# Kernel optimization log

Measured on AMD Instinct MI355X. Metric: run time of the kernel, lower is better.

## Reference

```python
import jax, jax.numpy as jnp
import numpy as np

C = 512
NUM_HEADS = 8
HEAD_DIM = 64
GROUPS = 32
EPS = 1e-5


def setup_inputs() -> dict:
    key = jax.random.key(0)
    ks = jax.random.split(key, 7)
    x = jax.random.normal(ks[0], (2, C, 64, 64), dtype=jnp.float32)
    norm_w = jnp.ones((C,), jnp.float32)
    norm_b = jnp.zeros((C,), jnp.float32)
    s1 = 1.0 / np.sqrt(C)
    qkv_w = jax.random.uniform(ks[1], (3 * C, C), jnp.float32, -s1, s1)
    qkv_b = jax.random.uniform(ks[2], (3 * C,), jnp.float32, -s1, s1)
    proj_w = jax.random.uniform(ks[3], (C, C), jnp.float32, -s1, s1)
    proj_b = jax.random.uniform(ks[4], (C,), jnp.float32, -s1, s1)
    return {"x": x, "norm_w": norm_w, "norm_b": norm_b,
            "qkv_w": qkv_w, "qkv_b": qkv_b,
            "proj_w": proj_w, "proj_b": proj_b}


def reference(x, norm_w, norm_b, qkv_w, qkv_b, proj_w, proj_b):
    b, c, h, w = x.shape
    n = h * w
    x_flat = x.reshape(b, c, n)
    # GroupNorm(32, C): stats over (channels-in-group, spatial)
    xg = x_flat.reshape(b, GROUPS, c // GROUPS, n)
    mean = xg.mean(axis=(2, 3), keepdims=True)
    var = xg.var(axis=(2, 3), keepdims=True)
    hn = ((xg - mean) * jax.lax.rsqrt(var + EPS)).reshape(b, c, n)
    hn = hn * norm_w[None, :, None] + norm_b[None, :, None]
    # 1x1 conv QKV = matmul over channel dim
    qkv = jnp.einsum('oc,bcn->bon', qkv_w, hn) + qkv_b[None, :, None]
    q, k, v = jnp.split(qkv, 3, axis=1)
    q = q.reshape(b, NUM_HEADS, HEAD_DIM, n)
    k = k.reshape(b, NUM_HEADS, HEAD_DIM, n)
    v = v.reshape(b, NUM_HEADS, HEAD_DIM, n)
    scale = HEAD_DIM ** (-0.5)
    attn = jnp.einsum('bhdn,bhdm->bhnm', q, k) * scale  # [b,H,N,N]
    attn = jax.nn.softmax(attn, axis=-1)
    out = jnp.einsum('bhnm,bhdm->bhdn', attn, v).reshape(b, c, n)
    out = jnp.einsum('oc,bcn->bon', proj_w, out) + proj_b[None, :, None]
    return (x_flat + out).reshape(b, c, h, w)
```

## Files before the change

### kernel.cpp

```cpp
#include <hip/hip_runtime.h>
#include <hip/hip_bf16.h>
#include <math.h>

#define BATCH 2
#define CCH   512
#define NSP   4096
#define NHEAD 8
#define HDIM  64
#define NGRP  32
#define CPG   16
#define EPSV  1e-5f
#define NSPLIT 2
#define MTN   (NSP / NSPLIT / 64)
#define SMSCALE 0.1803368801111204f

typedef __attribute__((ext_vector_type(8))) short short8;
typedef __attribute__((ext_vector_type(4))) short short4v;
typedef __attribute__((ext_vector_type(4))) float f32x4;
typedef __hip_bfloat16 bf16;

static __device__ __forceinline__ unsigned pk2(float a, float b) {
    return ((__float_as_uint(a) + 0x8000u) >> 16) |
           ((__float_as_uint(b) + 0x8000u) & 0xFFFF0000u);
}
static __device__ __forceinline__ unsigned pk1(float a) {
    return (__float_as_uint(a) + 0x8000u) >> 16;
}
static __device__ __forceinline__ float upk(unsigned u) {
    unsigned v = u << 16;
    return __uint_as_float(v);
}
static __device__ __forceinline__ float fexp2(float x) {
    return __builtin_amdgcn_exp2f(x);
}
static __device__ __forceinline__ void gload16(const bf16* g, bf16* l) {
    __builtin_amdgcn_global_load_lds(
        (const __attribute__((address_space(1))) unsigned*)g,
        (__attribute__((address_space(3))) unsigned*)l, 16, 0, 0);
}

__global__ __launch_bounds__(256) void prep0(const float* __restrict__ x,
                                             const float* __restrict__ qkvw,
                                             const float* __restrict__ pw,
                                             float* __restrict__ sbuf,
                                             bf16* __restrict__ wq, bf16* __restrict__ wp) {
    if (blockIdx.x < 1024) {
        const int bg = blockIdx.x >> 4, sub = blockIdx.x & 15;
        const float4* p = (const float4*)(x + (size_t)bg * (CPG * NSP)) +
                          (size_t)sub * (CPG * NSP / 4 / 16);
        float s = 0.f, ss = 0.f;
#pragma unroll
        for (int it = 0; it < 4; it++) {
            float4 v = p[it * 256 + threadIdx.x];
            s  += v.x + v.y + v.z + v.w;
            ss += v.x * v.x + v.y * v.y + v.z * v.z + v.w * v.w;
        }
        for (int o = 32; o > 0; o >>= 1) {
            s  += __shfl_down(s, o);
            ss += __shfl_down(ss, o);
        }
        __shared__ float shs[4], shss[4];
        const int wid = threadIdx.x >> 6, lane = threadIdx.x & 63;
        if (lane == 0) { shs[wid] = s; shss[wid] = ss; }
        __syncthreads();
        if (threadIdx.x == 0) {
            s  = shs[0] + shs[1] + shs[2] + shs[3];
            ss = shss[0] + shss[1] + shss[2] + shss[3];
            sbuf[bg * 16 + sub]        = s;
            sbuf[1024 + bg * 16 + sub] = ss;
        }
    } else {
        const int i = (blockIdx.x - 1024) * 256 + threadIdx.x;
        const int NQ = 1536 * 512 / 4;
        float4 v; bf16* dst; int di;
        if (i < NQ) { v = ((const float4*)qkvw)[i]; dst = wq; di = i; }
        else        { v = ((const float4*)pw)[i - NQ]; dst = wp; di = i - NQ; }
        uint2 o = {pk2(v.x, v.y), pk2(v.z, v.w)};
        *(uint2*)(dst + (size_t)di * 4) = o;
    }
}

__global__ __launch_bounds__(256) void gn_apply_t(const float* __restrict__ x,
                                                  const float* __restrict__ sbuf,
                                                  const float* __restrict__ nw,
                                                  const float* __restrict__ nb,
                                                  bf16* __restrict__ hnt) {
    __shared__ float Ls[64][68];
    __shared__ float Gmu[4], Grs[4];
    const int b  = blockIdx.z;
    const int c0 = blockIdx.y * 64;
    const int n0 = blockIdx.x * 64;
    const int t  = threadIdx.x;
    const int cl = t >> 4, n4 = (t & 15) * 4;
    if (t < 4) {
        const int bg = b * NGRP + (c0 >> 4) + t;
        float s = 0.f, ss = 0.f;
#pragma unroll
        for (int i = 0; i < 16; i++) {
            s  += sbuf[bg * 16 + i];
            ss += sbuf[1024 + bg * 16 + i];
        }
        const float invn = 1.f / (float)(CPG * NSP);
        const float mu = s * invn;
        Gmu[t] = mu;
        Grs[t] = rsqrtf(ss * invn - mu * mu + EPSV);
    }
    __syncthreads();
#pragma unroll
    for (int ph = 0; ph < 4; ph++) {
        const int c  = c0 + ph * 16 + cl;
        const float mu = Gmu[ph], rs = Grs[ph];
        const float sw = nw[c] * rs;
        const float sb = nb[c] - mu * sw;
        float4 v = *(const float4*)&x[((size_t)b * CCH + c) * NSP + n0 + n4];
        float4 o;
        o.x = v.x * sw + sb; o.y = v.y * sw + sb;
        o.z = v.z * sw + sb; o.w = v.w * sw + sb;
        *(float4*)&Ls[ph * 16 + cl][n4] = o;
    }
    __syncthreads();
#pragma unroll
    for (int ph = 0; ph < 2; ph++) {
        const int task = ph * 256 + t;
        const int nl = task & 63, cc = (task >> 6) * 8;
        uint4 o;
        o.x = pk2(Ls[cc + 0][nl], Ls[cc + 1][nl]);
        o.y = pk2(Ls[cc + 2][nl], Ls[cc + 3][nl]);
        o.z = pk2(Ls[cc + 4][nl], Ls[cc + 5][nl]);
        o.w = pk2(Ls[cc + 6][nl], Ls[cc + 7][nl]);
        *(uint4*)&hnt[((size_t)b * NSP + n0 + nl) * CCH + c0 + cc] = o;
    }
}

#define GEMM_STAGE(CUR)                                         \
    gload16(aSrc0, &As[CUR][(wave * 16) * 32]);                 \
    gload16(aSrc1, &As[CUR][(64 + wave * 16) * 32]);            \
    gload16(bSrc0, &Bs[CUR][(wave * 16) * 32]);                 \
    gload16(bSrc1, &Bs[CUR][(64 + wave * 16) * 32]);            \
    aSrc0 += 32; aSrc1 += 32; bSrc0 += 32; bSrc1 += 32;

#define GEMM_MAIN(Wptr, Xptr)                                                            \
    __shared__ __align__(16) bf16 As[2][128 * 32];                                       \
    __shared__ __align__(16) bf16 Bs[2][128 * 32];                                       \
    const int t = threadIdx.x, wave = t >> 6, lane = t & 63;                             \
    const int quad = lane >> 4, l15 = lane & 15;                                         \
    const int srow = lane >> 2, scol = (lane & 3) * 8;                                   \
    const int b   = blockIdx.z;                                                          \
    const int wm = wave >> 1, wn = wave & 1;                                             \
    const int m0w = blockIdx.y * 128 + wm * 64;                                          \
    const int n0w = blockIdx.x * 128 + wn * 64;                                          \
    const bf16* aSrc0 = Wptr + (size_t)(blockIdx.y * 128 + wave * 16 + srow) * 512 + scol; \
    const bf16* aSrc1 = aSrc0 + (size_t)64 * 512;                                        \
    const bf16* bSrc0 = Xptr + ((size_t)b * NSP + blockIdx.x * 128 + wave * 16 + srow) * 512 + scol; \
    const bf16* bSrc1 = bSrc0 + (size_t)64 * 512;                                        \
    f32x4 acc[4][4];                                                                     \
    _Pragma("unroll")                                                                    \
    for (int i = 0; i < 4; i++)                                                          \
        _Pragma("unroll")                                                                \
        for (int j = 0; j < 4; j++) acc[i][j] = (f32x4){0.f, 0.f, 0.f, 0.f};             \
    GEMM_STAGE(0)                                                                        \
    __syncthreads();                                                                     \
    _Pragma("unroll")                                                                    \
    for (int ks = 0; ks < 16; ks++) {                                                    \
        const int cur = ks & 1;                                                          \
        if (ks < 15) { GEMM_STAGE(cur ^ 1) }                                             \
        short8 af[4], bfr[4];                                                            \
        _Pragma("unroll")                                                                \
        for (int mf = 0; mf < 4; mf++)                                                   \
            af[mf] = *(const short8*)&As[cur][(wm * 64 + mf * 16 + l15) * 32 + quad * 8]; \
        _Pragma("unroll")                                                                \
        for (int nf = 0; nf < 4; nf++)                                                   \
            bfr[nf] = *(const short8*)&Bs[cur][(wn * 64 + nf * 16 + l15) * 32 + quad * 8]; \
        _Pragma("unroll")                                                                \
        for (int mf = 0; mf < 4; mf++)                                                   \
            _Pragma("unroll")                                                            \
            for (int nf = 0; nf < 4; nf++)                                               \
                acc[mf][nf] = __builtin_amdgcn_mfma_f32_16x16x32_bf16(af[mf], bfr[nf],   \
                                                                      acc[mf][nf], 0, 0, 0); \
        __syncthreads();                                                                 \
    }

__global__ __launch_bounds__(256) void gemm_qkv(const bf16* __restrict__ Wb,
                                                const bf16* __restrict__ Xt,
                                                const float* __restrict__ bias,
                                                bf16* __restrict__ qt, bf16* __restrict__ kt,
                                                bf16* __restrict__ vt) {
    GEMM_MAIN(Wb, Xt)

    const int sec = m0w >> 9, h = (m0w >> 6) & 7, bh = b * NHEAD + h;
    const float sm = (sec == 0) ? SMSCALE : 1.0f;
    float bi[4][4];
#pragma unroll
    for (int mf = 0; mf < 4; mf++)
#pragma unroll
        for (int r = 0; r < 4; r++) bi[mf][r] = bias[m0w + mf * 16 + quad * 4 + r];

    if (sec < 2) {
        bf16* dst = (sec == 0) ? qt : kt;
#pragma unroll
        for (int mf = 0; mf < 4; mf++)
#pragma unroll
            for (int nf = 0; nf < 4; nf++) {
                const int n = n0w + nf * 16 + l15;
                float v0 = (acc[mf][nf][0] + bi[mf][0]) * sm;
                float v1 = (acc[mf][nf][1] + bi[mf][1]) * sm;
                float v2 = (acc[mf][nf][2] + bi[mf][2]) * sm;
                float v3 = (acc[mf][nf][3] + bi[mf][3]) * sm;
                uint2 o = {pk2(v0, v1), pk2(v2, v3)};
                *(uint2*)(dst + ((size_t)bh * NSP + n) * HDIM + mf * 16 + quad * 4) = o;
            }
    } else {
#pragma unroll
        for (int mf = 0; mf < 4; mf++)
#pragma unroll
            for (int nf = 0; nf < 4; nf++)
#pragma unroll
                for (int r = 0; r < 4; r++) {
                    const float v = acc[mf][nf][r] + bi[mf][r];
                    const int n = n0w + nf * 16 + l15;
                    const int d = mf * 16 + quad * 4 + r;
                    unsigned u = pk1(v);
                    vt[((size_t)bh * HDIM + d) * NSP + n] = *(bf16*)&u;
                }
    }
}

__global__ __launch_bounds__(256) void gemm_proj(const bf16* __restrict__ Wb,
                                                 const bf16* __restrict__ Xt,
                                                 const float* __restrict__ bias,
                                                 const float* __restrict__ resid,
                                                 float* __restrict__ out) {
    GEMM_MAIN(Wb, Xt)

    float bi[4][4];
#pragma unroll
    for (int mf = 0; mf < 4; mf++)
#pragma unroll
        for (int r = 0; r < 4; r++) bi[mf][r] = bias[m0w + mf * 16 + quad * 4 + r];

    float* scratch = (float*)As;
    const int n0 = blockIdx.x * 128;
#pragma unroll
    for (int p = 0; p < 4; p++) {
        if (wm == (p >> 1)) {
#pragma unroll
            for (int ml = 0; ml < 2; ml++) {
                const int mf = (p & 1) * 2 + ml;
#pragma unroll
                for (int nf = 0; nf < 4; nf++)
#pragma unroll
                    for (int r = 0; r < 4; r++)
                        scratch[(ml * 16 + quad * 4 + r) * 128 + wn * 64 + nf * 16 + l15] =
                            acc[mf][nf][r] + bi[mf][r];
            }
        }
        __syncthreads();
#pragma unroll
        for (int i = 0; i < 4; i++) {
            const int idx = i * 256 + t;
            const int row = idx >> 5, c4 = idx & 31;
            const int m = blockIdx.y * 128 + p * 32 + row;
            const size_t off = ((size_t)b * CCH + m) * NSP + n0 + c4 * 4;
            float4 rv = *(const float4*)&resid[off];
            float4 sv = *(const float4*)&scratch[row * 128 + c4 * 4];
            float4 ov;
            ov.x = sv.x + rv.x; ov.y = sv.y + rv.y;
            ov.z = sv.z + rv.z; ov.w = sv.w + rv.w;
            *(float4*)&out[off] = ov;
        }
        __syncthreads();
    }
}

__global__ __launch_bounds__(256, 2) void attn10(const bf16* __restrict__ qt,
                                                 const bf16* __restrict__ kt,
                                                 const bf16* __restrict__ vt,
                                                 bf16* __restrict__ opart,
                                                 float* __restrict__ lpart) {
    __shared__ __align__(16) bf16 Ks[2][64][68];
    __shared__ __align__(16) bf16 Vs[2][64][68];
    const int t = threadIdx.x, wave = t >> 6, lane = t & 63;
    const int quad = lane >> 4, l15 = lane & 15;
    const int blk = blockIdx.x;
    const int xcd = blk & 7, slot = blk >> 3;
    const int qtile = slot & 15;
    const int grp = xcd + 8 * (slot >> 4);
    const int spl = grp & 1, bh = grp >> 1;
    const int b = bh >> 3, h = bh & 7;
    const int qb  = qtile * 256 + wave * 64;
    const int kb0 = spl * (NSP / NSPLIT);

    const bf16* Qb = qt + (size_t)bh * NSP * HDIM;

    const int trow = t >> 3;
    const int tcol = (t & 7) * 8;
    const bf16* kSrcA = kt + (size_t)bh * NSP * HDIM + (size_t)(kb0 + trow) * HDIM + tcol;
    const bf16* kSrcB = kSrcA + 32 * HDIM;
    const bf16* vSrcA = vt + (size_t)bh * HDIM * NSP + (size_t)trow * NSP + kb0 + tcol;
    const bf16* vSrcB = vSrcA + (size_t)32 * NSP;

    short8 qf[4][2];
#pragma unroll
    for (int qs = 0; qs < 4; qs++)
#pragma unroll
        for (int c = 0; c < 2; c++)
            qf[qs][c] = *(const short8*)(Qb + (size_t)(qb + qs * 16 + l15) * HDIM + c * 32 + quad * 8);

    short8 onesf;
    {
        const short one = (short)0x3F80;
        short8 o1 = {one, one, one, one, one, one, one, one};
        short8 zz = {0, 0, 0, 0, 0, 0, 0, 0};
        onesf = (l15 == 0) ? o1 : zz;
    }

    f32x4 o[4][4], ol[4];
#pragma unroll
    for (int qs = 0; qs < 4; qs++) {
        ol[qs] = (f32x4){0.f, 0.f, 0.f, 0.f};
#pragma unroll
        for (int ds = 0; ds < 4; ds++) o[qs][ds] = (f32x4){0.f, 0.f, 0.f, 0.f};
    }

    uint4 rKA, rKB, rVA, rVB;
#define ATTN_LOAD()                                         \
    rKA = *(const uint4*)kSrcA; kSrcA += 64 * HDIM;         \
    rKB = *(const uint4*)kSrcB; kSrcB += 64 * HDIM;         \
    rVA = *(const uint4*)vSrcA; vSrcA += 64;                \
    rVB = *(const uint4*)vSrcB; vSrcB += 64;
#define ATTN_STAGE(BUF)                                     \
    *(uint4*)&Ks[BUF][trow][tcol] = rKA;                    \
    *(uint4*)&Ks[BUF][32 + trow][tcol] = rKB;               \
    *(uint4*)&Vs[BUF][trow][tcol] = rVA;                    \
    *(uint4*)&Vs[BUF][32 + trow][tcol] = rVB;
#define ATTN_COMPUTE(BUF)                                                                \
    {                                                                                    \
        short8 kf[4][2], vf[4][2];                                                       \
        _Pragma("unroll")                                                                \
        for (int ms = 0; ms < 4; ms++)                                                   \
            _Pragma("unroll")                                                            \
            for (int c = 0; c < 2; c++)                                                  \
                kf[ms][c] = *(const short8*)&Ks[BUF][ms * 16 + l15][c * 32 + quad * 8];  \
        _Pragma("unroll")                                                                \
        for (int ds = 0; ds < 4; ds++)                                                   \
            _Pragma("unroll")                                                            \
            for (int c = 0; c < 2; c++)                                                  \
                vf[ds][c] = *(const short8*)&Vs[BUF][ds * 16 + l15][c * 32 + quad * 8];  \
        _Pragma("unroll")                                                                \
        for (int qs = 0; qs < 4; qs++) {                                                 \
            f32x4 s[4];                                                                  \
            __builtin_amdgcn_s_setprio(1);                                               \
            _Pragma("unroll")                                                            \
            for (int ms = 0; ms < 4; ms++) {                                             \
                f32x4 a = (f32x4){0.f, 0.f, 0.f, 0.f};                                   \
                a = __builtin_amdgcn_mfma_f32_16x16x32_bf16(kf[ms][0], qf[qs][0], a, 0, 0, 0); \
                a = __builtin_amdgcn_mfma_f32_16x16x32_bf16(kf[ms][1], qf[qs][1], a, 0, 0, 0); \
                s[ms] = a;                                                               \
            }                                                                            \
            __builtin_amdgcn_s_setprio(0);                                               \
            unsigned rr[4][2];                                                           \
            _Pragma("unroll")                                                            \
            for (int ms = 0; ms < 4; ms++) {                                             \
                float e0 = fexp2(s[ms][0]);                                              \
                float e1 = fexp2(s[ms][1]);                                              \
                float e2 = fexp2(s[ms][2]);                                              \
                float e3 = fexp2(s[ms][3]);                                              \
                asm("v_cvt_pk_bf16_f32 %0, %1, %2" : "=v"(rr[ms][0]) : "v"(e0), "v"(e1)); \
                asm("v_cvt_pk_bf16_f32 %0, %1, %2" : "=v"(rr[ms][1]) : "v"(e2), "v"(e3)); \
            }                                                                            \
            _Pragma("unroll")                                                            \
            for (int j = 0; j < 2; j++) {                                                \
                asm("v_permlane32_swap_b32 %0, %1" : "+v"(rr[0][j]), "+v"(rr[1][j]));    \
                asm("v_permlane32_swap_b32 %0, %1" : "+v"(rr[2][j]), "+v"(rr[3][j]));    \
            }                                                                            \
            _Pragma("unroll")                                                            \
            for (int j = 0; j < 2; j++) {                                                \
                asm("v_permlane16_swap_b32 %0, %1" : "+v"(rr[0][j]), "+v"(rr[1][j]));    \
                asm("v_permlane16_swap_b32 %0, %1" : "+v"(rr[2][j]), "+v"(rr[3][j]));    \
            }                                                                            \
            short8 pf0, pf1;                                                             \
            {                                                                            \
                unsigned* p0 = (unsigned*)&pf0;                                          \
                p0[0] = rr[0][0]; p0[1] = rr[0][1]; p0[2] = rr[1][0]; p0[3] = rr[1][1];  \
                unsigned* p1 = (unsigned*)&pf1;                                          \
                p1[0] = rr[2][0]; p1[1] = rr[2][1]; p1[2] = rr[3][0]; p1[3] = rr[3][1];  \
            }                                                                            \
            __builtin_amdgcn_s_setprio(1);                                               \
            _Pragma("unroll")                                                            \
            for (int ds = 0; ds < 4; ds++) {                                             \
                f32x4 a = o[qs][ds];                                                     \
                a = __builtin_amdgcn_mfma_f32_16x16x32_bf16(pf0, vf[ds][0], a, 0, 0, 0); \
                a = __builtin_amdgcn_mfma_f32_16x16x32_bf16(pf1, vf[ds][1], a, 0, 0, 0); \
                o[qs][ds] = a;                                                           \
            }                                                                            \
            {                                                                            \
                f32x4 a = ol[qs];                                                        \
                a = __builtin_amdgcn_mfma_f32_16x16x32_bf16(pf0, onesf, a, 0, 0, 0);     \
                a = __builtin_amdgcn_mfma_f32_16x16x32_bf16(pf1, onesf, a, 0, 0, 0);     \
                ol[qs] = a;                                                              \
            }                                                                            \
            __builtin_amdgcn_s_setprio(0);                                               \
        }                                                                                \
    }

    ATTN_LOAD()
    ATTN_STAGE(0)
    ATTN_LOAD()
    __syncthreads();

    for (int mt = 0; mt < MTN; mt += 2) {
        ATTN_STAGE(1)
        ATTN_LOAD()
        ATTN_COMPUTE(0)
        __syncthreads();
        ATTN_STAGE(0)
        ATTN_LOAD()
        ATTN_COMPUTE(1)
        __syncthreads();
    }
#undef ATTN_LOAD
#undef ATTN_STAGE
#undef ATTN_COMPUTE

#pragma unroll
    for (int qs = 0; qs < 4; qs++) {
#pragma unroll
        for (int ds = 0; ds < 4; ds++)
#pragma unroll
            for (int r = 0; r < 4; r++) {
                const int q = qb + qs * 16 + quad * 4 + r;
                unsigned u = pk1(o[qs][ds][r]);
                opart[((size_t)(spl * BATCH + b) * NSP + q) * CCH + h * 64 + ds * 16 + l15] =
                    *(bf16*)&u;
            }
        if (l15 == 0) {
#pragma unroll
            for (int r = 0; r < 4; r++) {
                const int q = qb + qs * 16 + quad * 4 + r;
                lpart[(((size_t)spl * BATCH + b) * NHEAD + h) * NSP + q] = ol[qs][r];
            }
        }
    }
}

__global__ __launch_bounds__(256) void attn_combine(const bf16* __restrict__ opart,
                                                    const float* __restrict__ lpart,
                                                    bf16* __restrict__ att_t) {
    const int idx = blockIdx.x * 256 + threadIdx.x;
    const int c8 = (idx & 63) * 8;
    const int n  = (idx >> 6) & 4095;
    const int b  = idx >> 18;
    const int h  = c8 >> 6;
    float l = 0.f;
#pragma unroll
    for (int s = 0; s < NSPLIT; s++)
        l += lpart[(((size_t)s * BATCH + b) * NHEAD + h) * NSP + n];
    const float inv = 1.f / l;
    float acc[8] = {};
#pragma unroll
    for (int s = 0; s < NSPLIT; s++) {
        uint4 u = *(const uint4*)&opart[((size_t)(s * BATCH + b) * NSP + n) * CCH + c8];
        acc[0] += upk(u.x); acc[1] += upk(u.x >> 16);
        acc[2] += upk(u.y); acc[3] += upk(u.y >> 16);
        acc[4] += upk(u.z); acc[5] += upk(u.z >> 16);
        acc[6] += upk(u.w); acc[7] += upk(u.w >> 16);
    }
    uint4 o;
    o.x = pk2(acc[0] * inv, acc[1] * inv);
    o.y = pk2(acc[2] * inv, acc[3] * inv);
    o.z = pk2(acc[4] * inv, acc[5] * inv);
    o.w = pk2(acc[6] * inv, acc[7] * inv);
    *(uint4*)&att_t[((size_t)b * NSP + n) * CCH + c8] = o;
}

extern "C" void kernel_launch(void* const* d_in, const int* in_sizes, int n_in,
                              void* d_out, int out_size, void* d_ws, size_t ws_size,
                              hipStream_t stream) {
    const float* x    = (const float*)d_in[0];
    const float* nw   = (const float*)d_in[1];
    const float* nb   = (const float*)d_in[2];
    const float* qkvw = (const float*)d_in[3];
    const float* qkvb = (const float*)d_in[4];
    const float* pw   = (const float*)d_in[5];
    const float* pb   = (const float*)d_in[6];
    float* out = (float*)d_out;
    char* ws   = (char*)d_ws;

    float* sbuf = (float*)ws;
    bf16* wq  = (bf16*)(ws + (size_t)1  * 1024 * 1024);
    bf16* wp  = (bf16*)(ws + (size_t)3  * 1024 * 1024);
    bf16* hnt = (bf16*)(ws + (size_t)4  * 1024 * 1024);
    bf16* qtb = (bf16*)(ws + (size_t)12 * 1024 * 1024);
    bf16* ktb = (bf16*)(ws + (size_t)20 * 1024 * 1024);
    bf16* vtb = (bf16*)(ws + (size_t)28 * 1024 * 1024);
    bf16* opart = (bf16*)(ws + (size_t)36 * 1024 * 1024);
    float* lpart = (float*)(ws + (size_t)56 * 1024 * 1024);
    bf16* att = hnt;

    hipLaunchKernelGGL(prep0, dim3(1024 + 1024), dim3(256), 0, stream,
                       x, qkvw, pw, sbuf, wq, wp);
    hipLaunchKernelGGL(gn_apply_t, dim3(NSP / 64, CCH / 64, BATCH), dim3(256), 0, stream,
                       x, sbuf, nw, nb, hnt);
    hipLaunchKernelGGL(gemm_qkv, dim3(NSP / 128, 1536 / 128, BATCH), dim3(256), 0, stream,
                       wq, hnt, qkvb, qtb, ktb, vtb);
    hipLaunchKernelGGL(attn10, dim3(512), dim3(256), 0, stream,
                       qtb, ktb, vtb, opart, lpart);
    hipLaunchKernelGGL(attn_combine, dim3(BATCH * NSP * CCH / 8 / 256), dim3(256), 0, stream,
                       opart, lpart, att);
    hipLaunchKernelGGL(gemm_proj, dim3(NSP / 128, CCH / 128, BATCH), dim3(256), 0, stream,
                       wp, att, pb, x, out);
}
```

Measured before the change: 201.8 us.

## Fuse split-attention combine into projection GEMM B-operand load

Removes the separate attn_combine kernel and instead has gemm_proj read both split partial outputs and their softmax denominators, combine and normalize them in registers, and write the bf16 result directly into the shared-memory B tile. The combined attention tensor no longer makes a round trip through global memory and one launch is dropped. In exchange, each proj block redoes the combine for its tile across all four M-blocks, so opart is read repeatedly. The B operand also switches from async global-to-LDS loads to register loads with explicit writes, which may add latency to the GEMM pipeline.

New measurement: 203.8 us. Within noise of the previous version (+1.0%).

```diff
diff --git a/kernel.cpp b/kernel.cpp
--- a/kernel.cpp
+++ b/kernel.cpp
@@ -139,53 +139,50 @@
     gload16(bSrc1, &Bs[CUR][(64 + wave * 16) * 32]);            \
     aSrc0 += 32; aSrc1 += 32; bSrc0 += 32; bSrc1 += 32;
 
-#define GEMM_MAIN(Wptr, Xptr)                                                            \
-    __shared__ __align__(16) bf16 As[2][128 * 32];                                       \
-    __shared__ __align__(16) bf16 Bs[2][128 * 32];                                       \
-    const int t = threadIdx.x, wave = t >> 6, lane = t & 63;                             \
-    const int quad = lane >> 4, l15 = lane & 15;                                         \
-    const int srow = lane >> 2, scol = (lane & 3) * 8;                                   \
-    const int b   = blockIdx.z;                                                          \
-    const int wm = wave >> 1, wn = wave & 1;                                             \
-    const int m0w = blockIdx.y * 128 + wm * 64;                                          \
-    const int n0w = blockIdx.x * 128 + wn * 64;                                          \
-    const bf16* aSrc0 = Wptr + (size_t)(blockIdx.y * 128 + wave * 16 + srow) * 512 + scol; \
-    const bf16* aSrc1 = aSrc0 + (size_t)64 * 512;                                        \
-    const bf16* bSrc0 = Xptr + ((size_t)b * NSP + blockIdx.x * 128 + wave * 16 + srow) * 512 + scol; \
-    const bf16* bSrc1 = bSrc0 + (size_t)64 * 512;                                        \
-    f32x4 acc[4][4];                                                                     \
-    _Pragma("unroll")                                                                    \
-    for (int i = 0; i < 4; i++)                                                          \
-        _Pragma("unroll")                                                                \
-        for (int j = 0; j < 4; j++) acc[i][j] = (f32x4){0.f, 0.f, 0.f, 0.f};             \
-    GEMM_STAGE(0)                                                                        \
-    __syncthreads();                                                                     \
-    _Pragma("unroll")                                                                    \
-    for (int ks = 0; ks < 16; ks++) {                                                    \
-        const int cur = ks & 1;                                                          \
-        if (ks < 15) { GEMM_STAGE(cur ^ 1) }                                             \
-        short8 af[4], bfr[4];                                                            \
-        _Pragma("unroll")                                                                \
-        for (int mf = 0; mf < 4; mf++)                                                   \
-            af[mf] = *(const short8*)&As[cur][(wm * 64 + mf * 16 + l15) * 32 + quad * 8]; \
-        _Pragma("unroll")                                                                \
-        for (int nf = 0; nf < 4; nf++)                                                   \
-            bfr[nf] = *(const short8*)&Bs[cur][(wn * 64 + nf * 16 + l15) * 32 + quad * 8]; \
-        _Pragma("unroll")                                                                \
-        for (int mf = 0; mf < 4; mf++)                                                   \
-            _Pragma("unroll")                                                            \
-            for (int nf = 0; nf < 4; nf++)                                               \
-                acc[mf][nf] = __builtin_amdgcn_mfma_f32_16x16x32_bf16(af[mf], bfr[nf],   \
-                                                                      acc[mf][nf], 0, 0, 0); \
-        __syncthreads();                                                                 \
-    }
-
 __global__ __launch_bounds__(256) void gemm_qkv(const bf16* __restrict__ Wb,
                                                 const bf16* __restrict__ Xt,
                                                 const float* __restrict__ bias,
                                                 bf16* __restrict__ qt, bf16* __restrict__ kt,
                                                 bf16* __restrict__ vt) {
-    GEMM_MAIN(Wb, Xt)
+    __shared__ __align__(16) bf16 As[2][128 * 32];
+    __shared__ __align__(16) bf16 Bs[2][128 * 32];
+    const int t = threadIdx.x, wave = t >> 6, lane = t & 63;
+    const int quad = lane >> 4, l15 = lane & 15;
+    const int srow = lane >> 2, scol = (lane & 3) * 8;
+    const int b   = blockIdx.z;
+    const int wm = wave >> 1, wn = wave & 1;
+    const int m0w = blockIdx.y * 128 + wm * 64;
+    const int n0w = blockIdx.x * 128 + wn * 64;
+    const bf16* aSrc0 = Wb + (size_t)(blockIdx.y * 128 + wave * 16 + srow) * 512 + scol;
+    const bf16* aSrc1 = aSrc0 + (size_t)64 * 512;
+    const bf16* bSrc0 = Xt + ((size_t)b * NSP + blockIdx.x * 128 + wave * 16 + srow) * 512 + scol;
+    const bf16* bSrc1 = bSrc0 + (size_t)64 * 512;
+    f32x4 acc[4][4];
+#pragma unroll
+    for (int i = 0; i < 4; i++)
+#pragma unroll
+        for (int j = 0; j < 4; j++) acc[i][j] = (f32x4){0.f, 0.f, 0.f, 0.f};
+    GEMM_STAGE(0)
+    __syncthreads();
+#pragma unroll
+    for (int ks = 0; ks < 16; ks++) {
+        const int cur = ks & 1;
+        if (ks < 15) { GEMM_STAGE(cur ^ 1) }
+        short8 af[4], bfr[4];
+#pragma unroll
+        for (int mf = 0; mf < 4; mf++)
+            af[mf] = *(const short8*)&As[cur][(wm * 64 + mf * 16 + l15) * 32 + quad * 8];
+#pragma unroll
+        for (int nf = 0; nf < 4; nf++)
+            bfr[nf] = *(const short8*)&Bs[cur][(wn * 64 + nf * 16 + l15) * 32 + quad * 8];
+#pragma unroll
+        for (int mf = 0; mf < 4; mf++)
+#pragma unroll
+            for (int nf = 0; nf < 4; nf++)
+                acc[mf][nf] = __builtin_amdgcn_mfma_f32_16x16x32_bf16(af[mf], bfr[nf],
+                                                                      acc[mf][nf], 0, 0, 0);
+        __syncthreads();
+    }
 
     const int sec = m0w >> 9, h = (m0w >> 6) & 7, bh = b * NHEAD + h;
     const float sm = (sec == 0) ? SMSCALE : 1.0f;
@@ -226,11 +223,98 @@
 }
 
 __global__ __launch_bounds__(256) void gemm_proj(const bf16* __restrict__ Wb,
-                                                 const bf16* __restrict__ Xt,
+                                                 const bf16* __restrict__ opart,
+                                                 const float* __restrict__ lpart,
                                                  const float* __restrict__ bias,
                                                  const float* __restrict__ resid,
                                                  float* __restrict__ out) {
-    GEMM_MAIN(Wb, Xt)
+    __shared__ __align__(16) bf16 As[2][128 * 32];
+    __shared__ __align__(16) bf16 Bs[2][128 * 32];
+    const int t = threadIdx.x, wave = t >> 6, lane = t & 63;
+    const int quad = lane >> 4, l15 = lane & 15;
+    const int srow = lane >> 2, scol = (lane & 3) * 8;
+    const int b   = blockIdx.z;
+    const int wm = wave >> 1, wn = wave & 1;
+    const int m0w = blockIdx.y * 128 + wm * 64;
+    const bf16* aSrc0 = Wb + (size_t)(blockIdx.y * 128 + wave * 16 + srow) * 512 + scol;
+    const bf16* aSrc1 = aSrc0 + (size_t)64 * 512;
+
+    const int rA   = blockIdx.x * 128 + (t >> 2);
+    const int rB   = rA + 64;
+    const int csub = (t & 3) * 8;
+    const bf16*  op0 = opart + (size_t)b * NSP * CCH;
+    const bf16*  op1 = opart + (size_t)(BATCH + b) * NSP * CCH;
+    const float* lp0 = lpart + (size_t)b * NHEAD * NSP;
+    const float* lp1 = lpart + (size_t)(BATCH + b) * NHEAD * NSP;
+
+    uint4 u0a, u1a, u0b, u1b;
+    float la, lb;
+#define PROJB_LOAD(KS)                                                          \
+    {                                                                           \
+        const int c8 = (KS) * 32 + csub;                                        \
+        const int hh = c8 >> 6;                                                 \
+        u0a = *(const uint4*)&op0[(size_t)rA * CCH + c8];                       \
+        u1a = *(const uint4*)&op1[(size_t)rA * CCH + c8];                       \
+        u0b = *(const uint4*)&op0[(size_t)rB * CCH + c8];                       \
+        u1b = *(const uint4*)&op1[(size_t)rB * CCH + c8];                       \
+        la = lp0[(size_t)hh * NSP + rA] + lp1[(size_t)hh * NSP + rA];           \
+        lb = lp0[(size_t)hh * NSP + rB] + lp1[(size_t)hh * NSP + rB];           \
+    }
+#define CMB(U0, U1, INV)                                                        \
+    pk2((upk(U0) + upk(U1)) * (INV), (upk((U0) >> 16) + upk((U1) >> 16)) * (INV))
+#define PROJB_WRITE(CUR)                                                        \
+    {                                                                           \
+        const float inva = 1.f / la, invb = 1.f / lb;                           \
+        uint4 w;                                                                \
+        w.x = CMB(u0a.x, u1a.x, inva); w.y = CMB(u0a.y, u1a.y, inva);           \
+        w.z = CMB(u0a.z, u1a.z, inva); w.w = CMB(u0a.w, u1a.w, inva);           \
+        *(uint4*)&Bs[CUR][(t >> 2) * 32 + csub] = w;                            \
+        w.x = CMB(u0b.x, u1b.x, invb); w.y = CMB(u0b.y, u1b.y, invb);           \
+        w.z = CMB(u0b.z, u1b.z, invb); w.w = CMB(u0b.w, u1b.w, invb);           \
+        *(uint4*)&Bs[CUR][(64 + (t >> 2)) * 32 + csub] = w;                     \
+    }
+
+    f32x4 acc[4][4];
+#pragma unroll
+    for (int i = 0; i < 4; i++)
+#pragma unroll
+        for (int j = 0; j < 4; j++) acc[i][j] = (f32x4){0.f, 0.f, 0.f, 0.f};
+
+    PROJB_LOAD(0)
+    gload16(aSrc0, &As[0][(wave * 16) * 32]);
+    gload16(aSrc1, &As[0][(64 + wave * 16) * 32]);
+    aSrc0 += 32; aSrc1 += 32;
+    PROJB_WRITE(0)
+    __syncthreads();
+
+#pragma unroll
+    for (int ks = 0; ks < 16; ks++) {
+        const int cur = ks & 1;
+        if (ks < 15) {
+            gload16(aSrc0, &As[cur ^ 1][(wave * 16) * 32]);
+            gload16(aSrc1, &As[cur ^ 1][(64 + wave * 16) * 32]);
+            aSrc0 += 32; aSrc1 += 32;
+            PROJB_LOAD(ks + 1)
+        }
+        short8 af[4], bfr[4];
+#pragma unroll
+        for (int mf = 0; mf < 4; mf++)
+            af[mf] = *(const short8*)&As[cur][(wm * 64 + mf * 16 + l15) * 32 + quad * 8];
+#pragma unroll
+        for (int nf = 0; nf < 4; nf++)
+            bfr[nf] = *(const short8*)&Bs[cur][(wn * 64 + nf * 16 + l15) * 32 + quad * 8];
+#pragma unroll
+        for (int mf = 0; mf < 4; mf++)
+#pragma unroll
+            for (int nf = 0; nf < 4; nf++)
+                acc[mf][nf] = __builtin_amdgcn_mfma_f32_16x16x32_bf16(af[mf], bfr[nf],
+                                                                      acc[mf][nf], 0, 0, 0);
+        if (ks < 15) { PROJB_WRITE(cur ^ 1) }
+        __syncthreads();
+    }
+#undef PROJB_LOAD
+#undef PROJB_WRITE
+#undef CMB
 
     float bi[4][4];
 #pragma unroll
@@ -443,36 +527,6 @@
     }
 }
 
-__global__ __launch_bounds__(256) void attn_combine(const bf16* __restrict__ opart,
-                                                    const float* __restrict__ lpart,
-                                                    bf16* __restrict__ att_t) {
-    const int idx = blockIdx.x * 256 + threadIdx.x;
-    const int c8 = (idx & 63) * 8;
-    const int n  = (idx >> 6) & 4095;
-    const int b  = idx >> 18;
-    const int h  = c8 >> 6;
-    float l = 0.f;
-#pragma unroll
-    for (int s = 0; s < NSPLIT; s++)
-        l += lpart[(((size_t)s * BATCH + b) * NHEAD + h) * NSP + n];
-    const float inv = 1.f / l;
-    float acc[8] = {};
-#pragma unroll
-    for (int s = 0; s < NSPLIT; s++) {
-        uint4 u = *(const uint4*)&opart[((size_t)(s * BATCH + b) * NSP + n) * CCH + c8];
-        acc[0] += upk(u.x); acc[1] += upk(u.x >> 16);
-        acc[2] += upk(u.y); acc[3] += upk(u.y >> 16);
-        acc[4] += upk(u.z); acc[5] += upk(u.z >> 16);
-        acc[6] += upk(u.w); acc[7] += upk(u.w >> 16);
-    }
-    uint4 o;
-    o.x = pk2(acc[0] * inv, acc[1] * inv);
-    o.y = pk2(acc[2] * inv, acc[3] * inv);
-    o.z = pk2(acc[4] * inv, acc[5] * inv);
-    o.w = pk2(acc[6] * inv, acc[7] * inv);
-    *(uint4*)&att_t[((size_t)b * NSP + n) * CCH + c8] = o;
-}
-
 extern "C" void kernel_launch(void* const* d_in, const int* in_sizes, int n_in,
                               void* d_out, int out_size, void* d_ws, size_t ws_size,
                               hipStream_t stream) {
@@ -495,7 +549,6 @@
     bf16* vtb = (bf16*)(ws + (size_t)28 * 1024 * 1024);
     bf16* opart = (bf16*)(ws + (size_t)36 * 1024 * 1024);
     float* lpart = (float*)(ws + (size_t)56 * 1024 * 1024);
-    bf16* att = hnt;
 
     hipLaunchKernelGGL(prep0, dim3(1024 + 1024), dim3(256), 0, stream,
                        x, qkvw, pw, sbuf, wq, wp);
@@ -505,8 +558,6 @@
                        wq, hnt, qkvb, qtb, ktb, vtb);
     hipLaunchKernelGGL(attn10, dim3(512), dim3(256), 0, stream,
                        qtb, ktb, vtb, opart, lpart);
-    hipLaunchKernelGGL(attn_combine, dim3(BATCH * NSP * CCH / 8 / 256), dim3(256), 0, stream,
-                       opart, lpart, att);
     hipLaunchKernelGGL(gemm_proj, dim3(NSP / 128, CCH / 128, BATCH), dim3(256), 0, stream,
-                       wp, att, pb, x, out);
-}
+                       wp, opart, lpart, pb, x, out);
+}
```
